# Optimization experiments

Measured on AMD Instinct MI355X. Metric: run time of the kernel, lower is better.

## Reference

```python
import jax, jax.numpy as jnp
import numpy as np

EPS = 1e-5

def bn_relu(x, g, b, leaky=0.0):
    # x: [B, C, N]; batch-norm over (batch, spatial) like torch train-mode BatchNorm1d
    m = x.mean((0, 2), keepdims=True)
    v = x.var((0, 2), keepdims=True)
    y = (x - m) * jax.lax.rsqrt(v + EPS) * g[None, :, None] + b[None, :, None]
    return jnp.where(y > 0, y, leaky * y)

def fps(xyz, npoint):
    # xyz: [B, N, 3] -> indices [B, npoint] (farthest point sampling, start at 0)
    B, N, _ = xyz.shape
    init_idx = jnp.zeros((B,), jnp.int32)
    d0 = jnp.full((B, N), 1e10, xyz.dtype)

    def step(carry, _):
        dists, last = carry
        p = jnp.take_along_axis(xyz, last[:, None, None], axis=1)  # [B,1,3]
        d = jnp.sum((xyz - p) ** 2, -1)                            # [B,N]
        dists = jnp.minimum(dists, d)
        nxt = jnp.argmax(dists, -1).astype(jnp.int32)
        return (dists, nxt), nxt

    (_, _), idxs = jax.lax.scan(step, (d0, init_idx), None, length=npoint - 1)
    return jnp.concatenate([init_idx[None, :], idxs], 0).T  # [B, npoint]

def sample_and_group(npoint, nsample, xyz, feat):
    # xyz: [B,N,3], feat: [B,N,C] -> new_xyz [B,S,3], new_feat [B,S,K,2C]
    fidx = fps(xyz, npoint)
    new_xyz = jnp.take_along_axis(xyz, fidx[:, :, None], axis=1)    # [B,S,3]
    center = jnp.take_along_axis(feat, fidx[:, :, None], axis=1)    # [B,S,C]
    # kNN of the S centers among all N points
    d = (jnp.sum(new_xyz ** 2, -1)[:, :, None]
         + jnp.sum(xyz ** 2, -1)[:, None, :]
         - 2.0 * jnp.einsum('bsc,bnc->bsn', new_xyz, xyz))          # [B,S,N]
    _, knn = jax.lax.top_k(-d, nsample)                              # [B,S,K]
    grouped = jnp.take_along_axis(feat[:, None, :, :], knn[..., None], axis=2)  # [B,S,K,C]
    gnorm = grouped - center[:, :, None, :]
    K = nsample
    new_feat = jnp.concatenate([gnorm, jnp.broadcast_to(center[:, :, None, :], gnorm.shape)], -1)
    return new_xyz, new_feat

def local_op(x, w1, g1, b1, w2, g2, b2):
    # x: [b, n, s, d] -> [b, out, n]
    b_, n, s, d = x.shape
    x = x.transpose(0, 1, 3, 2).reshape(b_ * n, d, s)   # [b*n, d, s]
    x1 = bn_relu(jnp.einsum('oc,bcs->bos', w1, x), g1, b1)
    x2 = bn_relu(jnp.einsum('oc,bcs->bos', w2, x1), g2, b2)
    x3 = x2.max(-1)                                      # adaptive_max_pool1d(.,1)
    return x3.reshape(b_, n, -1).transpose(0, 2, 1)

def setup_inputs() -> dict:
    key = jax.random.key(0)
    ks = jax.random.split(key, 16)
    f32 = jnp.float32
    B, N = 32, 1024
    inp = {
        'x': jax.random.normal(ks[0], (B, 6, N), f32),
        'w_c1': jax.random.normal(ks[1], (64, 6), f32) * 0.1,
        'g1': jnp.ones((64,), f32), 'b1': jnp.zeros((64,), f32),
        'w_c2': jax.random.normal(ks[2], (1024, 64), f32) * 0.05,
        'g2': jnp.ones((1024,), f32), 'b2': jnp.zeros((1024,), f32),
        'l0_w1': jax.random.normal(ks[3], (128, 128), f32) * 0.05,
        'l0_g1': jnp.ones((128,), f32), 'l0_b1': jnp.zeros((128,), f32),
        'l0_w2': jax.random.normal(ks[4], (128, 128), f32) * 0.05,
        'l0_g2': jnp.ones((128,), f32), 'l0_b2': jnp.zeros((128,), f32),
        'l1_w1': jax.random.normal(ks[5], (256, 256), f32) * 0.05,
        'l1_g1': jnp.ones((256,), f32), 'l1_b1': jnp.zeros((256,), f32),
        'l1_w2': jax.random.normal(ks[6], (256, 256), f32) * 0.05,
        'l1_g2': jnp.ones((256,), f32), 'l1_b2': jnp.zeros((256,), f32),
        'wf': jax.random.normal(ks[7], (512, 1280), f32) * 0.02,
        'gf': jnp.ones((512,), f32), 'bf': jnp.zeros((512,), f32),
    }
    return inp

def reference(x, w_c1, g1, b1, w_c2, g2, b2,
              l0_w1, l0_g1, l0_b1, l0_w2, l0_g2, l0_b2,
              l1_w1, l1_g1, l1_b1, l1_w2, l1_g2, l1_b2,
              wf, gf, bf):
    point_num = x.shape[2]
    stride = point_num // 256
    xyz = x[:, 0:3, :].transpose(0, 2, 1)                      # [B,N,3]
    h = bn_relu(jnp.einsum('oc,bcn->bon', w_c1, x), g1, b1)     # [B,64,N]
    x_skip = bn_relu(jnp.einsum('oc,bcn->bon', w_c2, h[:, :, ::stride]), g2, b2)  # [B,1024,256]
    feat = h.transpose(0, 2, 1)                                 # [B,N,64]
    new_xyz, nf = sample_and_group(512, 32, xyz, feat)          # nf: [B,512,32,128]
    f0 = local_op(nf, l0_w1, l0_g1, l0_b1, l0_w2, l0_g2, l0_b2) # [B,128,512]
    new_xyz, nf = sample_and_group(256, 32, new_xyz, f0.transpose(0, 2, 1))  # [B,256,32,256]
    f1 = local_op(nf, l1_w1, l1_g1, l1_b1, l1_w2, l1_g2, l1_b2) # [B,256,256]
    f1 = jnp.concatenate([f1, x_skip], 1)                        # [B,1280,256]
    res = bn_relu(jnp.einsum('oc,bcn->bon', wf, f1), gf, bf, leaky=0.2)  # [B,512,256]
    return res
```

## Files before the change

kernel.cpp:

```cpp
#include <hip/hip_runtime.h>
#include <stdint.h>

typedef unsigned int u32;
typedef unsigned short u16;
typedef __attribute__((ext_vector_type(8))) short bf16x8;
typedef __attribute__((ext_vector_type(4))) float f32x4;

#define DEV __device__ __forceinline__
#define BN_EPS 1e-5f

DEV float bf2f(u16 u){ return __uint_as_float(((u32)u) << 16); }
DEV u16 f2bf(float f){ u32 x = __float_as_uint(f); return (u16)((x + 0x7FFFu + ((x >> 16) & 1u)) >> 16); }

template<int CTRL, int RMASK, bool MAXOP>
DEV void dpp_step(float& d, u32& i){
  int ds = __float_as_int(d);
  int is = (int)i;
  int dn_ = __builtin_amdgcn_update_dpp(ds, ds, CTRL, RMASK, 0xf, false);
  int in_ = __builtin_amdgcn_update_dpp(is, is, CTRL, RMASK, 0xf, false);
  float dn = __int_as_float(dn_);
  u32 ii = (u32)in_;
  bool take = MAXOP ? (dn > d || (dn == d && ii < i))
                    : (dn < d || (dn == d && ii < i));
  if (take){ d = dn; i = ii; }
}

template<bool MAXOP>
DEV u32 dpp_arg_reduce(float& d, u32& i){
  dpp_step<0x111, 0xf, MAXOP>(d, i);
  dpp_step<0x112, 0xf, MAXOP>(d, i);
  dpp_step<0x114, 0xf, MAXOP>(d, i);
  dpp_step<0x118, 0xf, MAXOP>(d, i);
  dpp_step<0x142, 0xa, MAXOP>(d, i);
  dpp_step<0x143, 0xc, MAXOP>(d, i);
  return (u32)__builtin_amdgcn_readlane((int)i, 63);
}

__global__ void kfb(float* out, int n, float code){
  int i = blockIdx.x * 256 + threadIdx.x;
  if (i < n) out[i] = (i == 0) ? code : 0.f;
}

__global__ void kcast_bf(const float* __restrict__ src, int rows, int cols, int srcStride, int colOff,
                         u16* __restrict__ dst){
  int i = blockIdx.x * 256 + threadIdx.x;
  if (i >= rows * cols) return;
  int r = i / cols, c = i - r * cols;
  dst[r * cols + c] = f2bf(src[r * srcStride + colOff + c]);
}

__global__ __launch_bounds__(256) void kA_stats(const float* __restrict__ x, const float* __restrict__ w,
                                                const float* __restrict__ g, const float* __restrict__ b,
                                                float* __restrict__ sc, float* __restrict__ sh){
  int c = blockIdx.x, t = threadIdx.x;
  float wr[6];
#pragma unroll
  for (int j = 0; j < 6; ++j) wr[j] = w[c * 6 + j];
  float s = 0.f, ss = 0.f;
  for (int i = t; i < 32768; i += 256){
    int bb = i >> 10, n = i & 1023;
    const float* xb = x + bb * 6144 + n;
    float y = 0.f;
#pragma unroll
    for (int j = 0; j < 6; ++j) y += wr[j] * xb[j * 1024];
    s += y; ss += y * y;
  }
  __shared__ float rs[256], rq[256];
  rs[t] = s; rq[t] = ss; __syncthreads();
  for (int k = 128; k >= 1; k >>= 1){
    if (t < k){ rs[t] += rs[t + k]; rq[t] += rq[t + k]; }
    __syncthreads();
  }
  if (t == 0){
    float m = rs[0] * (1.f / 32768.f), e2 = rq[0] * (1.f / 32768.f);
    float var = e2 - m * m; if (var < 0.f) var = 0.f;
    float scv = g[c] * rsqrtf(var + BN_EPS);
    sc[c] = scv; sh[c] = b[c] - m * scv;
  }
}

__global__ __launch_bounds__(256) void kA_feat(const float* __restrict__ x, const float* __restrict__ w,
                                               const float* __restrict__ sc, const float* __restrict__ sh,
                                               u16* __restrict__ featT){
  int b = blockIdx.x >> 2, t = threadIdx.x;
  int n = ((blockIdx.x & 3) << 8) + t;
  __shared__ float wl[384], scl[64], shl[64];
  for (int u = t; u < 384; u += 256) wl[u] = w[u];
  if (t < 64){ scl[t] = sc[t]; shl[t] = sh[t]; }
  __syncthreads();
  float v[6];
  const float* xb = x + b * 6144 + n;
#pragma unroll
  for (int j = 0; j < 6; ++j) v[j] = xb[j * 1024];
  u32* row = (u32*)(featT + ((size_t)b * 1024 + n) * 64);
#pragma unroll
  for (int c2 = 0; c2 < 32; ++c2){
    float y0 = 0.f, y1 = 0.f;
#pragma unroll
    for (int j = 0; j < 6; ++j){
      y0 += wl[(2 * c2) * 6 + j] * v[j];
      y1 += wl[(2 * c2 + 1) * 6 + j] * v[j];
    }
    y0 = fmaxf(scl[2 * c2] * y0 + shl[2 * c2], 0.f);
    y1 = fmaxf(scl[2 * c2 + 1] * y1 + shl[2 * c2 + 1], 0.f);
    row[c2] = (u32)f2bf(y0) | ((u32)f2bf(y1) << 16);
  }
}

__global__ __launch_bounds__(256) void kxskip_pre(const u16* __restrict__ featT, const float* __restrict__ w2,
                                                  u16* __restrict__ xpre){
  int b = blockIdx.x >> 4, ot = blockIdx.x & 15, m = threadIdx.x;
  __shared__ float w2s[64][65];
  for (int u = threadIdx.x; u < 64 * 64; u += 256){
    int o = u >> 6, c = u & 63;
    w2s[o][c] = w2[(size_t)(ot * 64 + o) * 64 + c];
  }
  __syncthreads();
  float feat[64];
  const uint4* fr = (const uint4*)(featT + ((size_t)b * 1024 + 4 * m) * 64);
#pragma unroll
  for (int q = 0; q < 8; ++q){
    uint4 pv = fr[q];
    u32 wv[4] = {pv.x, pv.y, pv.z, pv.w};
#pragma unroll
    for (int h = 0; h < 4; ++h){
      feat[q * 8 + 2 * h]     = bf2f((u16)(wv[h] & 0xffff));
      feat[q * 8 + 2 * h + 1] = bf2f((u16)(wv[h] >> 16));
    }
  }
  u16* xb = xpre + ((size_t)b * 1024 + ot * 64) * 256 + m;
  for (int o = 0; o < 64; ++o){
    float acc = 0.f;
#pragma unroll
    for (int c = 0; c < 64; ++c) acc += w2s[o][c] * feat[c];
    xb[(size_t)o * 256] = f2bf(acc);
  }
}

__global__ __launch_bounds__(256) void kxskip_stats(const u16* __restrict__ xpre, const float* __restrict__ g,
                                                    const float* __restrict__ b, float* __restrict__ sc,
                                                    float* __restrict__ sh){
  int o = blockIdx.x, t = threadIdx.x;
  float s = 0.f, ss = 0.f;
  for (int i = t; i < 8192; i += 256){
    int bb = i >> 8, m = i & 255;
    float v = bf2f(xpre[((size_t)bb * 1024 + o) * 256 + m]);
    s += v; ss += v * v;
  }
  __shared__ float rs[256], rq[256];
  rs[t] = s; rq[t] = ss; __syncthreads();
  for (int k = 128; k >= 1; k >>= 1){
    if (t < k){ rs[t] += rs[t + k]; rq[t] += rq[t + k]; }
    __syncthreads();
  }
  if (t == 0){
    float m = rs[0] * (1.f / 8192.f), e2 = rq[0] * (1.f / 8192.f);
    float var = e2 - m * m; if (var < 0.f) var = 0.f;
    float scv = g[o] * rsqrtf(var + BN_EPS);
    sc[o] = scv; sh[o] = b[o] - m * scv;
  }
}

template<int NPTS, int NSAMP, int PSTRIDE>
__global__ __launch_bounds__(64) void kfps(const float* __restrict__ px_, const float* __restrict__ py_,
                                           const float* __restrict__ pz_, int bstride,
                                           int* __restrict__ fidx, float* __restrict__ nxyz){
  constexpr int PPL = NPTS / 64;
  __shared__ float sx[NPTS], sy[NPTS], sz[NPTS];
  int b = blockIdx.x, lane = threadIdx.x;
  float dd[PPL];
#pragma unroll
  for (int j = 0; j < PPL; ++j){
    int p = j * 64 + lane;
    sx[p] = px_[(size_t)b * bstride + p * PSTRIDE];
    sy[p] = py_[(size_t)b * bstride + p * PSTRIDE];
    sz[p] = pz_[(size_t)b * bstride + p * PSTRIDE];
    dd[j] = 1e10f;
  }
  __syncthreads();
  float cx = sx[0], cy = sy[0], cz = sz[0];
  if (lane == 0){
    fidx[(size_t)b * NSAMP] = 0;
    nxyz[(size_t)b * NSAMP * 3 + 0] = cx;
    nxyz[(size_t)b * NSAMP * 3 + 1] = cy;
    nxyz[(size_t)b * NSAMP * 3 + 2] = cz;
  }
  for (int s = 1; s < NSAMP; ++s){
    float bd = -1.f; u32 bi = 0;
#pragma unroll
    for (int j = 0; j < PPL; ++j){
      int p = j * 64 + lane;
      float dx = __fsub_rn(sx[p], cx);
      float dy = __fsub_rn(sy[p], cy);
      float dz = __fsub_rn(sz[p], cz);
      float d = __fadd_rn(__fadd_rn(__fmul_rn(dx, dx), __fmul_rn(dy, dy)), __fmul_rn(dz, dz));
      float v = fminf(dd[j], d);
      dd[j] = v;
      if (v > bd){ bd = v; bi = (u32)p; }
    }
    u32 win = dpp_arg_reduce<true>(bd, bi);
    cx = sx[win]; cy = sy[win]; cz = sz[win];
    if (lane == 0){
      fidx[(size_t)b * NSAMP + s] = (int)win;
      nxyz[((size_t)b * NSAMP + s) * 3 + 0] = cx;
      nxyz[((size_t)b * NSAMP + s) * 3 + 1] = cy;
      nxyz[((size_t)b * NSAMP + s) * 3 + 2] = cz;
    }
  }
}

template<int NPTS, int SOUT>
__global__ __launch_bounds__(256) void kknn(const float* __restrict__ px_, const float* __restrict__ py_,
                                            const float* __restrict__ pz_, int bstride, int pstride,
                                            const float* __restrict__ cxyz, int* __restrict__ knn){
  constexpr int PPL = NPTS / 64;
  int wid = blockIdx.x * 4 + (threadIdx.x >> 6);
  int lane = threadIdx.x & 63;
  int b = wid / SOUT, s = wid - b * SOUT;
  const float* cb = cxyz + ((size_t)b * SOUT + s) * 3;
  float cx = cb[0], cy = cb[1], cz = cb[2];
  float csq = __fadd_rn(__fadd_rn(__fmul_rn(cx, cx), __fmul_rn(cy, cy)), __fmul_rn(cz, cz));
  float kd[PPL];
#pragma unroll
  for (int j = 0; j < PPL; ++j){
    int p = j * 64 + lane;
    float xx = px_[(size_t)b * bstride + p * pstride];
    float yy = py_[(size_t)b * bstride + p * pstride];
    float zz = pz_[(size_t)b * bstride + p * pstride];
    float psq = __fadd_rn(__fadd_rn(__fmul_rn(xx, xx), __fmul_rn(yy, yy)), __fmul_rn(zz, zz));
    float dot = __fadd_rn(__fadd_rn(__fmul_rn(cx, xx), __fmul_rn(cy, yy)), __fmul_rn(cz, zz));
    kd[j] = __fsub_rn(__fadd_rn(csq, psq), __fmul_rn(2.f, dot));
  }
  int* outp = knn + ((size_t)b * SOUT + s) * 32;
  for (int k = 0; k < 32; ++k){
    float bd = kd[0]; u32 bi = (u32)lane;
#pragma unroll
    for (int j = 1; j < PPL; ++j){
      u32 p = (u32)(j * 64 + lane);
      if (kd[j] < bd){ bd = kd[j]; bi = p; }
    }
    u32 win = dpp_arg_reduce<false>(bd, bi);
    if (lane == 0) outp[k] = (int)win;
#pragma unroll
    for (int j = 0; j < PPL; ++j) if ((u32)(j * 64 + lane) == win) kd[j] = 3e38f;
  }
}

template<int CIN, int C, int NPTSRC, int SLOG>
__global__ __launch_bounds__(256) void kgm_pre(const u16* __restrict__ featSrc, const int* __restrict__ knnIdx,
                                               const int* __restrict__ fidx, const float* __restrict__ w1f,
                                               const u16* __restrict__ w1bf,
                                               u16* __restrict__ pre1, float* __restrict__ part){
  constexpr int MT  = C / 64;
  constexpr int KS1 = CIN / 32;
  constexpr int P1  = CIN + 8;
  int g = blockIdx.x, t = threadIdx.x, b = g >> SLOG;
  int l = t & 63, wv = t >> 6;
  int lg = l >> 4, ln = l & 15;

  __shared__ int   idxs[32];
  __shared__ float cen[CIN];
  __shared__ float bias[C];
  __shared__ u16   gsT[32][P1];

  if (t < 32) idxs[t] = knnIdx[(size_t)g * 32 + t];
  for (int u = t; u < CIN; u += 256) cen[u] = bf2f(featSrc[((size_t)(b * NPTSRC + fidx[g])) * CIN + u]);
  __syncthreads();

  for (int u = t; u < 32 * CIN / 8; u += 256){
    int k = u & 31, c8 = u >> 5;
    uint4 pv = *(const uint4*)(featSrc + ((size_t)(b * NPTSRC + idxs[k])) * CIN + c8 * 8);
    u32 wvv[4] = {pv.x, pv.y, pv.z, pv.w};
    u32 outw[4];
#pragma unroll
    for (int h = 0; h < 4; ++h){
      float a0 = bf2f((u16)(wvv[h] & 0xffff)) - cen[c8 * 8 + 2 * h];
      float a1 = bf2f((u16)(wvv[h] >> 16))    - cen[c8 * 8 + 2 * h + 1];
      outw[h] = (u32)f2bf(a0) | ((u32)f2bf(a1) << 16);
    }
    *(uint4*)&gsT[k][c8 * 8] = make_uint4(outw[0], outw[1], outw[2], outw[3]);
  }
  if (t < C){
    const float* wr = w1f + (size_t)t * (2 * CIN) + CIN;
    float bs = 0.f;
#pragma unroll 4
    for (int c = 0; c < CIN; ++c) bs += wr[c] * cen[c];
    bias[t] = bs;
  }
  __syncthreads();

  f32x4 acc[MT][2];
#pragma unroll
  for (int mt = 0; mt < MT; ++mt){ acc[mt][0] = (f32x4)0.f; acc[mt][1] = (f32x4)0.f; }
#pragma unroll
  for (int ks = 0; ks < KS1; ++ks){
    int c0 = ks * 32 + lg * 8;
    bf16x8 bfr0 = *(const bf16x8*)&gsT[ln][c0];
    bf16x8 bfr1 = *(const bf16x8*)&gsT[16 + ln][c0];
#pragma unroll
    for (int mt = 0; mt < MT; ++mt){
      int o0 = wv * (C / 4) + mt * 16;
      bf16x8 afr = *(const bf16x8*)(w1bf + (size_t)(o0 + ln) * CIN + c0);
      acc[mt][0] = __builtin_amdgcn_mfma_f32_16x16x32_bf16(afr, bfr0, acc[mt][0], 0, 0, 0);
      acc[mt][1] = __builtin_amdgcn_mfma_f32_16x16x32_bf16(afr, bfr1, acc[mt][1], 0, 0, 0);
    }
  }

#pragma unroll
  for (int mt = 0; mt < MT; ++mt){
    int obase = wv * (C / 4) + mt * 16 + lg * 4;
#pragma unroll
    for (int j = 0; j < 4; ++j){
      int o = obase + j;
      float bv = bias[o];
      float vA = acc[mt][0][j] + bv, vB = acc[mt][1][j] + bv;
      u16* pp = pre1 + ((size_t)g * C + o) * 32 + ln;
      pp[0]  = f2bf(vA);
      pp[16] = f2bf(vB);
      float s = vA + vB, ss = vA * vA + vB * vB;
#pragma unroll
      for (int mk = 1; mk < 16; mk <<= 1){ s += __shfl_xor(s, mk, 64); ss += __shfl_xor(ss, mk, 64); }
      if (ln == 0){
        part[((size_t)g * C + o) * 2 + 0] = s;
        part[((size_t)g * C + o) * 2 + 1] = ss;
      }
    }
  }
}

template<int C>
__global__ __launch_bounds__(256) void kgm_post(const u16* __restrict__ pre1,
                                                const float* __restrict__ sc1g, const float* __restrict__ sh1g,
                                                const u16* __restrict__ w2bf, const float* __restrict__ gp,
                                                float* __restrict__ part, float* __restrict__ pooledPre){
  constexpr int MT  = C / 64;
  constexpr int KS2 = C / 32;
  constexpr int P2  = C + 8;
  int g = blockIdx.x, t = threadIdx.x;
  int l = t & 63, wv = t >> 6;
  int lg = l >> 4, ln = l & 15;

  __shared__ u16   act2[32][P2];
  __shared__ float sc1s[C], sh1s[C];
  for (int u = t; u < C; u += 256){ sc1s[u] = sc1g[u]; sh1s[u] = sh1g[u]; }
  __syncthreads();

  for (int u = t; u < C * 4; u += 256){
    uint4 pv = *(const uint4*)(pre1 + (size_t)g * C * 32 + (size_t)u * 8);
    int o = u >> 2, k0 = (u & 3) << 3;
    float s1 = sc1s[o], h1 = sh1s[o];
    u32 wvv[4] = {pv.x, pv.y, pv.z, pv.w};
#pragma unroll
    for (int h = 0; h < 4; ++h){
      float a0 = fmaxf(s1 * bf2f((u16)(wvv[h] & 0xffff)) + h1, 0.f);
      float a1 = fmaxf(s1 * bf2f((u16)(wvv[h] >> 16))    + h1, 0.f);
      act2[k0 + 2 * h][o]     = f2bf(a0);
      act2[k0 + 2 * h + 1][o] = f2bf(a1);
    }
  }
  __syncthreads();

  f32x4 acc[MT][2];
#pragma unroll
  for (int mt = 0; mt < MT; ++mt){ acc[mt][0] = (f32x4)0.f; acc[mt][1] = (f32x4)0.f; }
#pragma unroll
  for (int ks = 0; ks < KS2; ++ks){
    int c0 = ks * 32 + lg * 8;
    bf16x8 bfr0 = *(const bf16x8*)&act2[ln][c0];
    bf16x8 bfr1 = *(const bf16x8*)&act2[16 + ln][c0];
#pragma unroll
    for (int mt = 0; mt < MT; ++mt){
      int o0 = wv * (C / 4) + mt * 16;
      bf16x8 afr = *(const bf16x8*)(w2bf + (size_t)(o0 + ln) * C + c0);
      acc[mt][0] = __builtin_amdgcn_mfma_f32_16x16x32_bf16(afr, bfr0, acc[mt][0], 0, 0, 0);
      acc[mt][1] = __builtin_amdgcn_mfma_f32_16x16x32_bf16(afr, bfr1, acc[mt][1], 0, 0, 0);
    }
  }

#pragma unroll
  for (int mt = 0; mt < MT; ++mt){
    int obase = wv * (C / 4) + mt * 16 + lg * 4;
#pragma unroll
    for (int j = 0; j < 4; ++j){
      float vA = acc[mt][0][j], vB = acc[mt][1][j];
      float s = vA + vB, ss = vA * vA + vB * vB;
      float mx = fmaxf(vA, vB), mn = fminf(vA, vB);
#pragma unroll
      for (int mk = 1; mk < 16; mk <<= 1){
        s += __shfl_xor(s, mk, 64); ss += __shfl_xor(ss, mk, 64);
        mx = fmaxf(mx, __shfl_xor(mx, mk, 64)); mn = fminf(mn, __shfl_xor(mn, mk, 64));
      }
      if (ln == 0){
        int o = obase + j;
        part[((size_t)g * C + o) * 2 + 0] = s;
        part[((size_t)g * C + o) * 2 + 1] = ss;
        pooledPre[(size_t)g * C + o] = (gp[o] >= 0.f) ? mx : mn;
      }
    }
  }
}

template<int C, int NG>
__global__ __launch_bounds__(256) void kstats_part(const float* __restrict__ part, const float* __restrict__ g_,
                                                   const float* __restrict__ b_, float* __restrict__ sc,
                                                   float* __restrict__ sh){
  int o = blockIdx.x, t = threadIdx.x;
  float s = 0.f, ss = 0.f;
  for (int i = t; i < NG; i += 256){
    s  += part[((size_t)i * C + o) * 2 + 0];
    ss += part[((size_t)i * C + o) * 2 + 1];
  }
  __shared__ float rs[256], rq[256];
  rs[t] = s; rq[t] = ss; __syncthreads();
  for (int k = 128; k >= 1; k >>= 1){
    if (t < k){ rs[t] += rs[t + k]; rq[t] += rq[t + k]; }
    __syncthreads();
  }
  if (t == 0){
    const float inv_n = 1.f / (float)(NG * 32);
    float m = rs[0] * inv_n, e2 = rq[0] * inv_n;
    float var = e2 - m * m; if (var < 0.f) var = 0.f;
    float scv = g_[o] * rsqrtf(var + BN_EPS);
    sc[o] = scv; sh[o] = b_[o] - m * scv;
  }
}

__global__ void kpool_fin1(const float* __restrict__ pooledPre, const float* __restrict__ sc,
                           const float* __restrict__ sh, u16* __restrict__ f0feat){
  int i = blockIdx.x * 256 + threadIdx.x;
  if (i >= 16384 * 128) return;
  int o = i & 127;
  float v = sc[o] * pooledPre[i] + sh[o];
  f0feat[i] = f2bf(fmaxf(v, 0.f));
}

__global__ void kpool_finT(const float* __restrict__ pooledPre, const float* __restrict__ sc,
                           const float* __restrict__ sh, u16* __restrict__ f1T){
  int i = blockIdx.x * 256 + threadIdx.x;
  if (i >= 8192 * 256) return;
  int gg = i >> 8, o = i & 255;
  int b = gg >> 8, s = gg & 255;
  float v = sc[o] * pooledPre[i] + sh[o];
  f1T[((size_t)(b * 256 + o)) * 256 + s] = f2bf(fmaxf(v, 0.f));
}

__global__ __launch_bounds__(256) void kfinal8(const u16* __restrict__ f1T, const u16* __restrict__ xpre,
                                               const float* __restrict__ scS, const float* __restrict__ shS,
                                               const float* __restrict__ wf, u16* __restrict__ finpre){
  int b = blockIdx.x >> 6, ot = blockIdx.x & 63, m = threadIdx.x;
  int o0 = ot * 8;
  const float* wb = wf + (size_t)o0 * 1280;
  float acc[8];
#pragma unroll
  for (int j = 0; j < 8; ++j) acc[j] = 0.f;
  const u16* fb = f1T + (size_t)b * 256 * 256 + m;
  for (int k = 0; k < 256; ++k){
    float v = bf2f(fb[(size_t)k * 256]);
#pragma unroll
    for (int j = 0; j < 8; ++j) acc[j] = fmaf(wb[(size_t)j * 1280 + k], v, acc[j]);
  }
  const u16* xb = xpre + (size_t)b * 1024 * 256 + m;
  for (int k = 0; k < 1024; ++k){
    float xv = bf2f(xb[(size_t)k * 256]);
    float v = fmaxf(scS[k] * xv + shS[k], 0.f);
#pragma unroll
    for (int j = 0; j < 8; ++j) acc[j] = fmaf(wb[(size_t)j * 1280 + 256 + k], v, acc[j]);
  }
#pragma unroll
  for (int j = 0; j < 8; ++j)
    finpre[((size_t)b * 512 + o0 + j) * 256 + m] = f2bf(acc[j]);
}

__global__ __launch_bounds__(256) void kstats_fin(const u16* __restrict__ finpre, const float* __restrict__ g,
                                                  const float* __restrict__ b, float* __restrict__ sc,
                                                  float* __restrict__ sh){
  int o = blockIdx.x, t = threadIdx.x;
  float s = 0.f, ss = 0.f;
  for (int i = t; i < 8192; i += 256){
    int bb = i >> 8, m = i & 255;
    float v = bf2f(finpre[((size_t)bb * 512 + o) * 256 + m]);
    s += v; ss += v * v;
  }
  __shared__ float rs[256], rq[256];
  rs[t] = s; rq[t] = ss; __syncthreads();
  for (int k = 128; k >= 1; k >>= 1){
    if (t < k){ rs[t] += rs[t + k]; rq[t] += rq[t + k]; }
    __syncthreads();
  }
  if (t == 0){
    float m = rs[0] * (1.f / 8192.f), e2 = rq[0] * (1.f / 8192.f);
    float var = e2 - m * m; if (var < 0.f) var = 0.f;
    float scv = g[o] * rsqrtf(var + BN_EPS);
    sc[o] = scv; sh[o] = b[o] - m * scv;
  }
}

__global__ void kapply(const u16* __restrict__ finpre, const float* __restrict__ sc,
                       const float* __restrict__ sh, float* __restrict__ out){
  int i = blockIdx.x * 256 + threadIdx.x;
  if (i >= 32 * 512 * 256) return;
  int o = (i >> 8) & 511;
  float v = sc[o] * bf2f(finpre[i]) + sh[o];
  out[i] = v > 0.f ? v : 0.2f * v;
}

extern "C" void kernel_launch(void* const* d_in, const int* in_sizes, int n_in,
                              void* d_out, int out_size, void* d_ws, size_t ws_size,
                              hipStream_t stream){
  const float* x    = (const float*)d_in[0];
  const float* w_c1 = (const float*)d_in[1];
  const float* g1   = (const float*)d_in[2];
  const float* b1   = (const float*)d_in[3];
  const float* w_c2 = (const float*)d_in[4];
  const float* g2   = (const float*)d_in[5];
  const float* b2   = (const float*)d_in[6];
  const float* l0w1 = (const float*)d_in[7];
  const float* l0g1 = (const float*)d_in[8];
  const float* l0b1 = (const float*)d_in[9];
  const float* l0w2 = (const float*)d_in[10];
  const float* l0g2 = (const float*)d_in[11];
  const float* l0b2 = (const float*)d_in[12];
  const float* l1w1 = (const float*)d_in[13];
  const float* l1g1 = (const float*)d_in[14];
  const float* l1b1 = (const float*)d_in[15];
  const float* l1w2 = (const float*)d_in[16];
  const float* l1g2 = (const float*)d_in[17];
  const float* l1b2 = (const float*)d_in[18];
  const float* wf   = (const float*)d_in[19];
  const float* gf   = (const float*)d_in[20];
  const float* bfp  = (const float*)d_in[21];
  float* out = (float*)d_out;

  char* ws = (char*)d_ws;
  size_t cur = 0;
  auto alloc = [&](size_t bytes) -> char* {
    char* p = ws + cur;
    cur += (bytes + 255) & ~(size_t)255;
    return p;
  };
  float* sc1  = (float*)alloc(64 * 4);    float* sh1  = (float*)alloc(64 * 4);
  float* scSK = (float*)alloc(1024 * 4);  float* shSK = (float*)alloc(1024 * 4);
  float* scA1 = (float*)alloc(128 * 4);   float* shA1 = (float*)alloc(128 * 4);
  float* scA2 = (float*)alloc(128 * 4);   float* shA2 = (float*)alloc(128 * 4);
  float* scC1 = (float*)alloc(256 * 4);   float* shC1 = (float*)alloc(256 * 4);
  float* scC2 = (float*)alloc(256 * 4);   float* shC2 = (float*)alloc(256 * 4);
  float* scF  = (float*)alloc(512 * 4);   float* shF  = (float*)alloc(512 * 4);
  u16* w1bf1 = (u16*)alloc((size_t)128 * 64 * 2);
  u16* w2bf1 = (u16*)alloc((size_t)128 * 128 * 2);
  u16* w1bf2 = (u16*)alloc((size_t)256 * 128 * 2);
  u16* w2bf2 = (u16*)alloc((size_t)256 * 256 * 2);
  u16*   featT  = (u16*)  alloc((size_t)32 * 1024 * 64 * 2);
  u16*   xpre   = (u16*)  alloc((size_t)32 * 1024 * 256 * 2);
  int*   fidx1  = (int*)  alloc((size_t)32 * 512 * 4);
  float* nxyz1  = (float*)alloc((size_t)32 * 512 * 3 * 4);
  int*   knn1   = (int*)  alloc((size_t)32 * 512 * 32 * 4);
  int*   fidx2  = (int*)  alloc((size_t)32 * 256 * 4);
  float* nxyz2  = (float*)alloc((size_t)32 * 256 * 3 * 4);
  int*   knn2   = (int*)  alloc((size_t)32 * 256 * 32 * 4);
  u16*   pre1   = (u16*)  alloc((size_t)16384 * 128 * 32 * 2);
  float* part   = (float*)alloc((size_t)16384 * 128 * 2 * 4);
  float* pooledPre = (float*)alloc((size_t)16384 * 128 * 4);
  u16*   f0feat = (u16*)  alloc((size_t)16384 * 128 * 2);
  u16*   f1T    = (u16*)  alloc((size_t)32 * 256 * 256 * 2);
  u16*   finpre = (u16*)  alloc((size_t)32 * 512 * 256 * 2);

  if (cur > ws_size){
    float code = -1000.f - (float)(ws_size >> 20);
    kfb<<<(out_size + 255) / 256, 256, 0, stream>>>(out, out_size, code);
    return;
  }

  kcast_bf<<<(128 * 64 + 255) / 256, 256, 0, stream>>>(l0w1, 128, 64, 128, 0, w1bf1);
  kcast_bf<<<(128 * 128 + 255) / 256, 256, 0, stream>>>(l0w2, 128, 128, 128, 0, w2bf1);
  kcast_bf<<<(256 * 128 + 255) / 256, 256, 0, stream>>>(l1w1, 256, 128, 256, 0, w1bf2);
  kcast_bf<<<(256 * 256 + 255) / 256, 256, 0, stream>>>(l1w2, 256, 256, 256, 0, w2bf2);

  kA_stats<<<64, 256, 0, stream>>>(x, w_c1, g1, b1, sc1, sh1);
  kA_feat<<<128, 256, 0, stream>>>(x, w_c1, sc1, sh1, featT);

  kxskip_pre<<<512, 256, 0, stream>>>(featT, w_c2, xpre);
  kxskip_stats<<<1024, 256, 0, stream>>>(xpre, g2, b2, scSK, shSK);

  kfps<1024, 512, 1><<<32, 64, 0, stream>>>(x, x + 1024, x + 2048, 6144, fidx1, nxyz1);
  kknn<1024, 512><<<32 * 512 / 4, 256, 0, stream>>>(x, x + 1024, x + 2048, 6144, 1, nxyz1, knn1);

  kgm_pre<64, 128, 1024, 9><<<16384, 256, 0, stream>>>(featT, knn1, fidx1, l0w1, w1bf1, pre1, part);
  kstats_part<128, 16384><<<128, 256, 0, stream>>>(part, l0g1, l0b1, scA1, shA1);
  kgm_post<128><<<16384, 256, 0, stream>>>(pre1, scA1, shA1, w2bf1, l0g2, part, pooledPre);
  kstats_part<128, 16384><<<128, 256, 0, stream>>>(part, l0g2, l0b2, scA2, shA2);
  kpool_fin1<<<8192, 256, 0, stream>>>(pooledPre, scA2, shA2, f0feat);

  kfps<512, 256, 3><<<32, 64, 0, stream>>>(nxyz1, nxyz1 + 1, nxyz1 + 2, 1536, fidx2, nxyz2);
  kknn<512, 256><<<32 * 256 / 4, 256, 0, stream>>>(nxyz1, nxyz1 + 1, nxyz1 + 2, 1536, 3, nxyz2, knn2);

  kgm_pre<128, 256, 512, 8><<<8192, 256, 0, stream>>>(f0feat, knn2, fidx2, l1w1, w1bf2, pre1, part);
  kstats_part<256, 8192><<<256, 256, 0, stream>>>(part, l1g1, l1b1, scC1, shC1);
  kgm_post<256><<<8192, 256, 0, stream>>>(pre1, scC1, shC1, w2bf2, l1g2, part, pooledPre);
  kstats_part<256, 8192><<<256, 256, 0, stream>>>(part, l1g2, l1b2, scC2, shC2);
  kpool_finT<<<8192, 256, 0, stream>>>(pooledPre, scC2, shC2, f1T);

  kfinal8<<<2048, 256, 0, stream>>>(f1T, xpre, scSK, shSK, wf, finpre);
  kstats_fin<<<512, 256, 0, stream>>>(finpre, gf, bfp, scF, shF);
  kapply<<<16384, 256, 0, stream>>>(finpre, scF, shF, out);
}
```

Measured before the change: 1.818 ms.

## Spread farthest point sampling across four waves per batch with cross-wave argmax

The FPS kernel now runs one 256-thread block per batch instead of a single 64-lane wave, so each lane handles a quarter as many points per iteration. Each wave does a DPP argmax reduction, and the four wave results are merged through double-buffered shared memory with one barrier per sample step. Points are stored as float4 in shared memory so each point is read with a single load. The serial per-step cost shrinks, but a block barrier is added on every sampled point, which could eat part of the gain for the smaller 512-point stage.

```diff
diff --git a/kernel.cpp b/kernel.cpp
--- a/kernel.cpp
+++ b/kernel.cpp
@@ -26,14 +26,22 @@
 }
 
 template<bool MAXOP>
-DEV u32 dpp_arg_reduce(float& d, u32& i){
+DEV void dpp_arg_reduce_vi(float& d, u32& i, float& outd, u32& outi){
   dpp_step<0x111, 0xf, MAXOP>(d, i);
   dpp_step<0x112, 0xf, MAXOP>(d, i);
   dpp_step<0x114, 0xf, MAXOP>(d, i);
   dpp_step<0x118, 0xf, MAXOP>(d, i);
   dpp_step<0x142, 0xa, MAXOP>(d, i);
   dpp_step<0x143, 0xc, MAXOP>(d, i);
-  return (u32)__builtin_amdgcn_readlane((int)i, 63);
+  outi = (u32)__builtin_amdgcn_readlane((int)i, 63);
+  outd = __int_as_float(__builtin_amdgcn_readlane(__float_as_int(d), 63));
+}
+
+template<bool MAXOP>
+DEV u32 dpp_arg_reduce(float& d, u32& i){
+  float od; u32 oi;
+  dpp_arg_reduce_vi<MAXOP>(d, i, od, oi);
+  return oi;
 }
 
 __global__ void kfb(float* out, int n, float code){
@@ -162,50 +170,67 @@
 }
 
 template<int NPTS, int NSAMP, int PSTRIDE>
-__global__ __launch_bounds__(64) void kfps(const float* __restrict__ px_, const float* __restrict__ py_,
-                                           const float* __restrict__ pz_, int bstride,
-                                           int* __restrict__ fidx, float* __restrict__ nxyz){
-  constexpr int PPL = NPTS / 64;
-  __shared__ float sx[NPTS], sy[NPTS], sz[NPTS];
-  int b = blockIdx.x, lane = threadIdx.x;
+__global__ __launch_bounds__(256) void kfps4(const float* __restrict__ px_, const float* __restrict__ py_,
+                                             const float* __restrict__ pz_, int bstride,
+                                             int* __restrict__ fidx, float* __restrict__ nxyz){
+  constexpr int PPL = NPTS / 256;
+  __shared__ float4 pts[NPTS];
+  __shared__ float rbd[2][4];
+  __shared__ u32   rbi[2][4];
+  int b = blockIdx.x, t = threadIdx.x;
+  int wv = t >> 6;
   float dd[PPL];
 #pragma unroll
   for (int j = 0; j < PPL; ++j){
-    int p = j * 64 + lane;
-    sx[p] = px_[(size_t)b * bstride + p * PSTRIDE];
-    sy[p] = py_[(size_t)b * bstride + p * PSTRIDE];
-    sz[p] = pz_[(size_t)b * bstride + p * PSTRIDE];
+    int p = j * 256 + t;
+    pts[p] = make_float4(px_[(size_t)b * bstride + p * PSTRIDE],
+                         py_[(size_t)b * bstride + p * PSTRIDE],
+                         pz_[(size_t)b * bstride + p * PSTRIDE], 0.f);
     dd[j] = 1e10f;
   }
   __syncthreads();
-  float cx = sx[0], cy = sy[0], cz = sz[0];
-  if (lane == 0){
+  float4 c0 = pts[0];
+  float cx = c0.x, cy = c0.y, cz = c0.z;
+  if (t == 0){
     fidx[(size_t)b * NSAMP] = 0;
     nxyz[(size_t)b * NSAMP * 3 + 0] = cx;
     nxyz[(size_t)b * NSAMP * 3 + 1] = cy;
     nxyz[(size_t)b * NSAMP * 3 + 2] = cz;
   }
+  int buf = 0;
   for (int s = 1; s < NSAMP; ++s){
     float bd = -1.f; u32 bi = 0;
 #pragma unroll
     for (int j = 0; j < PPL; ++j){
-      int p = j * 64 + lane;
-      float dx = __fsub_rn(sx[p], cx);
-      float dy = __fsub_rn(sy[p], cy);
-      float dz = __fsub_rn(sz[p], cz);
+      int p = j * 256 + t;
+      float4 pt = pts[p];
+      float dx = __fsub_rn(pt.x, cx);
+      float dy = __fsub_rn(pt.y, cy);
+      float dz = __fsub_rn(pt.z, cz);
       float d = __fadd_rn(__fadd_rn(__fmul_rn(dx, dx), __fmul_rn(dy, dy)), __fmul_rn(dz, dz));
       float v = fminf(dd[j], d);
       dd[j] = v;
       if (v > bd){ bd = v; bi = (u32)p; }
     }
-    u32 win = dpp_arg_reduce<true>(bd, bi);
-    cx = sx[win]; cy = sy[win]; cz = sz[win];
-    if (lane == 0){
-      fidx[(size_t)b * NSAMP + s] = (int)win;
+    float wbd; u32 wbi;
+    dpp_arg_reduce_vi<true>(bd, bi, wbd, wbi);
+    if ((t & 63) == 0){ rbd[buf][wv] = wbd; rbi[buf][wv] = wbi; }
+    __syncthreads();
+    float Bd = rbd[buf][0]; u32 Bi = rbi[buf][0];
+#pragma unroll
+    for (int w = 1; w < 4; ++w){
+      float od = rbd[buf][w]; u32 oi = rbi[buf][w];
+      if (od > Bd || (od == Bd && oi < Bi)){ Bd = od; Bi = oi; }
+    }
+    float4 cw = pts[Bi];
+    cx = cw.x; cy = cw.y; cz = cw.z;
+    if (t == 0){
+      fidx[(size_t)b * NSAMP + s] = (int)Bi;
       nxyz[((size_t)b * NSAMP + s) * 3 + 0] = cx;
       nxyz[((size_t)b * NSAMP + s) * 3 + 1] = cy;
       nxyz[((size_t)b * NSAMP + s) * 3 + 2] = cz;
     }
+    buf ^= 1;
   }
 }
 
@@ -581,7 +606,7 @@
   kxskip_pre<<<512, 256, 0, stream>>>(featT, w_c2, xpre);
   kxskip_stats<<<1024, 256, 0, stream>>>(xpre, g2, b2, scSK, shSK);
 
-  kfps<1024, 512, 1><<<32, 64, 0, stream>>>(x, x + 1024, x + 2048, 6144, fidx1, nxyz1);
+  kfps4<1024, 512, 1><<<32, 256, 0, stream>>>(x, x + 1024, x + 2048, 6144, fidx1, nxyz1);
   kknn<1024, 512><<<32 * 512 / 4, 256, 0, stream>>>(x, x + 1024, x + 2048, 6144, 1, nxyz1, knn1);
 
   kgm_pre<64, 128, 1024, 9><<<16384, 256, 0, stream>>>(featT, knn1, fidx1, l0w1, w1bf1, pre1, part);
@@ -590,7 +615,7 @@
   kstats_part<128, 16384><<<128, 256, 0, stream>>>(part, l0g2, l0b2, scA2, shA2);
   kpool_fin1<<<8192, 256, 0, stream>>>(pooledPre, scA2, shA2, f0feat);
 
-  kfps<512, 256, 3><<<32, 64, 0, stream>>>(nxyz1, nxyz1 + 1, nxyz1 + 2, 1536, fidx2, nxyz2);
+  kfps4<512, 256, 3><<<32, 256, 0, stream>>>(nxyz1, nxyz1 + 1, nxyz1 + 2, 1536, fidx2, nxyz2);
   kknn<512, 256><<<32 * 256 / 4, 256, 0, stream>>>(nxyz1, nxyz1 + 1, nxyz1 + 2, 1536, 3, nxyz2, knn2);
 
   kgm_pre<128, 256, 512, 8><<<8192, 256, 0, stream>>>(f0feat, knn2, fidx2, l1w1, w1bf2, pre1, part);
```

After: 1.926 ms. 6.0% more time.

## Overlap serial FPS with independent GEMM work via fused launches; cheaper DPP argmax

Applied to the files above, without the earlier changes.

The two farthest-point-sampling passes, which are serial single-wave loops on 32 blocks, now share a launch with independent work: the first FPS runs alongside the x_skip projection, and the second FPS runs alongside the first grouped-MLP pre-activation kernel. Because FPS2 depends only on nxyz1, it can start early instead of waiting behind stage-0 work. The DPP argmax/argmin reduction is rewritten as a float max/min reduction, a readlane broadcast, and then a min-index reduction, replacing paired compare-and-select steps. In exchange, FPS blocks now hold 256-thread slots with 192 idle threads, and the kgm_pre body shares a kernel with the FPS shared-memory footprint, which may reduce occupancy for the large grid.

```diff
diff --git a/kernel.cpp b/kernel.cpp
--- a/kernel.cpp
+++ b/kernel.cpp
@@ -12,28 +12,43 @@
 DEV float bf2f(u16 u){ return __uint_as_float(((u32)u) << 16); }
 DEV u16 f2bf(float f){ u32 x = __float_as_uint(f); return (u16)((x + 0x7FFFu + ((x >> 16) & 1u)) >> 16); }
 
-template<int CTRL, int RMASK, bool MAXOP>
-DEV void dpp_step(float& d, u32& i){
-  int ds = __float_as_int(d);
-  int is = (int)i;
-  int dn_ = __builtin_amdgcn_update_dpp(ds, ds, CTRL, RMASK, 0xf, false);
-  int in_ = __builtin_amdgcn_update_dpp(is, is, CTRL, RMASK, 0xf, false);
-  float dn = __int_as_float(dn_);
-  u32 ii = (u32)in_;
-  bool take = MAXOP ? (dn > d || (dn == d && ii < i))
-                    : (dn < d || (dn == d && ii < i));
-  if (take){ d = dn; i = ii; }
+template<int CTRL, int RMASK>
+DEV float dppf(float v){
+  int r = __builtin_amdgcn_update_dpp(__float_as_int(v), __float_as_int(v), CTRL, RMASK, 0xf, false);
+  return __int_as_float(r);
+}
+template<int CTRL, int RMASK>
+DEV u32 dppu(u32 v){
+  return (u32)__builtin_amdgcn_update_dpp((int)v, (int)v, CTRL, RMASK, 0xf, false);
 }
 
 template<bool MAXOP>
-DEV u32 dpp_arg_reduce(float& d, u32& i){
-  dpp_step<0x111, 0xf, MAXOP>(d, i);
-  dpp_step<0x112, 0xf, MAXOP>(d, i);
-  dpp_step<0x114, 0xf, MAXOP>(d, i);
-  dpp_step<0x118, 0xf, MAXOP>(d, i);
-  dpp_step<0x142, 0xa, MAXOP>(d, i);
-  dpp_step<0x143, 0xc, MAXOP>(d, i);
-  return (u32)__builtin_amdgcn_readlane((int)i, 63);
+DEV u32 arg_reduce2(float bd, u32 bi){
+  float m = bd;
+  if (MAXOP){
+    m = fmaxf(m, dppf<0x111, 0xf>(m));
+    m = fmaxf(m, dppf<0x112, 0xf>(m));
+    m = fmaxf(m, dppf<0x114, 0xf>(m));
+    m = fmaxf(m, dppf<0x118, 0xf>(m));
+    m = fmaxf(m, dppf<0x142, 0xa>(m));
+    m = fmaxf(m, dppf<0x143, 0xc>(m));
+  } else {
+    m = fminf(m, dppf<0x111, 0xf>(m));
+    m = fminf(m, dppf<0x112, 0xf>(m));
+    m = fminf(m, dppf<0x114, 0xf>(m));
+    m = fminf(m, dppf<0x118, 0xf>(m));
+    m = fminf(m, dppf<0x142, 0xa>(m));
+    m = fminf(m, dppf<0x143, 0xc>(m));
+  }
+  float M = __int_as_float(__builtin_amdgcn_readlane(__float_as_int(m), 63));
+  u32 key = (bd == M) ? bi : 0xFFFFFFFFu;
+  key = min(key, dppu<0x111, 0xf>(key));
+  key = min(key, dppu<0x112, 0xf>(key));
+  key = min(key, dppu<0x114, 0xf>(key));
+  key = min(key, dppu<0x118, 0xf>(key));
+  key = min(key, dppu<0x142, 0xa>(key));
+  key = min(key, dppu<0x143, 0xc>(key));
+  return (u32)__builtin_amdgcn_readlane((int)key, 63);
 }
 
 __global__ void kfb(float* out, int n, float code){
@@ -107,9 +122,58 @@
   }
 }
 
-__global__ __launch_bounds__(256) void kxskip_pre(const u16* __restrict__ featT, const float* __restrict__ w2,
-                                                  u16* __restrict__ xpre){
-  int b = blockIdx.x >> 4, ot = blockIdx.x & 15, m = threadIdx.x;
+template<int NPTS, int NSAMP, int PSTRIDE>
+DEV void fps_body(const float* __restrict__ px_, const float* __restrict__ py_,
+                  const float* __restrict__ pz_, int bstride,
+                  int* __restrict__ fidx, float* __restrict__ nxyz, int b){
+  constexpr int PPL = NPTS / 64;
+  __shared__ float sx[NPTS], sy[NPTS], sz[NPTS];
+  int t = threadIdx.x;
+  for (int p = t; p < NPTS; p += 256){
+    sx[p] = px_[(size_t)b * bstride + p * PSTRIDE];
+    sy[p] = py_[(size_t)b * bstride + p * PSTRIDE];
+    sz[p] = pz_[(size_t)b * bstride + p * PSTRIDE];
+  }
+  __syncthreads();
+  if (t >= 64) return;
+  int lane = t;
+  float dd[PPL];
+#pragma unroll
+  for (int j = 0; j < PPL; ++j) dd[j] = 1e10f;
+  float cx = sx[0], cy = sy[0], cz = sz[0];
+  if (lane == 0){
+    fidx[(size_t)b * NSAMP] = 0;
+    nxyz[(size_t)b * NSAMP * 3 + 0] = cx;
+    nxyz[(size_t)b * NSAMP * 3 + 1] = cy;
+    nxyz[(size_t)b * NSAMP * 3 + 2] = cz;
+  }
+  for (int s = 1; s < NSAMP; ++s){
+    float bd = -1.f; u32 bi = 0;
+#pragma unroll
+    for (int j = 0; j < PPL; ++j){
+      int p = j * 64 + lane;
+      float dx = __fsub_rn(sx[p], cx);
+      float dy = __fsub_rn(sy[p], cy);
+      float dz = __fsub_rn(sz[p], cz);
+      float d = __fadd_rn(__fadd_rn(__fmul_rn(dx, dx), __fmul_rn(dy, dy)), __fmul_rn(dz, dz));
+      float v = fminf(dd[j], d);
+      dd[j] = v;
+      if (v > bd){ bd = v; bi = (u32)p; }
+    }
+    u32 win = arg_reduce2<true>(bd, bi);
+    cx = sx[win]; cy = sy[win]; cz = sz[win];
+    if (lane == 0){
+      fidx[(size_t)b * NSAMP + s] = (int)win;
+      nxyz[((size_t)b * NSAMP + s) * 3 + 0] = cx;
+      nxyz[((size_t)b * NSAMP + s) * 3 + 1] = cy;
+      nxyz[((size_t)b * NSAMP + s) * 3 + 2] = cz;
+    }
+  }
+}
+
+DEV void xskip_body(const u16* __restrict__ featT, const float* __restrict__ w2,
+                    u16* __restrict__ xpre, int bi){
+  int b = bi >> 4, ot = bi & 15, m = threadIdx.x;
   __shared__ float w2s[64][65];
   for (int u = threadIdx.x; u < 64 * 64; u += 256){
     int o = u >> 6, c = u & 63;
@@ -134,6 +198,17 @@
 #pragma unroll
     for (int c = 0; c < 64; ++c) acc += w2s[o][c] * feat[c];
     xb[(size_t)o * 256] = f2bf(acc);
+  }
+}
+
+__global__ __launch_bounds__(256) void kfused1(const float* __restrict__ x,
+                                               const u16* __restrict__ featT, const float* __restrict__ w2,
+                                               u16* __restrict__ xpre,
+                                               int* __restrict__ fidx1, float* __restrict__ nxyz1){
+  if (blockIdx.x < 32){
+    fps_body<1024, 512, 1>(x, x + 1024, x + 2048, 6144, fidx1, nxyz1, blockIdx.x);
+  } else {
+    xskip_body(featT, w2, xpre, blockIdx.x - 32);
   }
 }
 
@@ -158,54 +233,6 @@
     float var = e2 - m * m; if (var < 0.f) var = 0.f;
     float scv = g[o] * rsqrtf(var + BN_EPS);
     sc[o] = scv; sh[o] = b[o] - m * scv;
-  }
-}
-
-template<int NPTS, int NSAMP, int PSTRIDE>
-__global__ __launch_bounds__(64) void kfps(const float* __restrict__ px_, const float* __restrict__ py_,
-                                           const float* __restrict__ pz_, int bstride,
-                                           int* __restrict__ fidx, float* __restrict__ nxyz){
-  constexpr int PPL = NPTS / 64;
-  __shared__ float sx[NPTS], sy[NPTS], sz[NPTS];
-  int b = blockIdx.x, lane = threadIdx.x;
-  float dd[PPL];
-#pragma unroll
-  for (int j = 0; j < PPL; ++j){
-    int p = j * 64 + lane;
-    sx[p] = px_[(size_t)b * bstride + p * PSTRIDE];
-    sy[p] = py_[(size_t)b * bstride + p * PSTRIDE];
-    sz[p] = pz_[(size_t)b * bstride + p * PSTRIDE];
-    dd[j] = 1e10f;
-  }
-  __syncthreads();
-  float cx = sx[0], cy = sy[0], cz = sz[0];
-  if (lane == 0){
-    fidx[(size_t)b * NSAMP] = 0;
-    nxyz[(size_t)b * NSAMP * 3 + 0] = cx;
-    nxyz[(size_t)b * NSAMP * 3 + 1] = cy;
-    nxyz[(size_t)b * NSAMP * 3 + 2] = cz;
-  }
-  for (int s = 1; s < NSAMP; ++s){
-    float bd = -1.f; u32 bi = 0;
-#pragma unroll
-    for (int j = 0; j < PPL; ++j){
-      int p = j * 64 + lane;
-      float dx = __fsub_rn(sx[p], cx);
-      float dy = __fsub_rn(sy[p], cy);
-      float dz = __fsub_rn(sz[p], cz);
-      float d = __fadd_rn(__fadd_rn(__fmul_rn(dx, dx), __fmul_rn(dy, dy)), __fmul_rn(dz, dz));
-      float v = fminf(dd[j], d);
-      dd[j] = v;
-      if (v > bd){ bd = v; bi = (u32)p; }
-    }
-    u32 win = dpp_arg_reduce<true>(bd, bi);
-    cx = sx[win]; cy = sy[win]; cz = sz[win];
-    if (lane == 0){
-      fidx[(size_t)b * NSAMP + s] = (int)win;
-      nxyz[((size_t)b * NSAMP + s) * 3 + 0] = cx;
-      nxyz[((size_t)b * NSAMP + s) * 3 + 1] = cy;
-      nxyz[((size_t)b * NSAMP + s) * 3 + 2] = cz;
-    }
   }
 }
 
@@ -239,7 +266,7 @@
       u32 p = (u32)(j * 64 + lane);
       if (kd[j] < bd){ bd = kd[j]; bi = p; }
     }
-    u32 win = dpp_arg_reduce<false>(bd, bi);
+    u32 win = arg_reduce2<false>(bd, bi);
     if (lane == 0) outp[k] = (int)win;
 #pragma unroll
     for (int j = 0; j < PPL; ++j) if ((u32)(j * 64 + lane) == win) kd[j] = 3e38f;
@@ -247,14 +274,14 @@
 }
 
 template<int CIN, int C, int NPTSRC, int SLOG>
-__global__ __launch_bounds__(256) void kgm_pre(const u16* __restrict__ featSrc, const int* __restrict__ knnIdx,
-                                               const int* __restrict__ fidx, const float* __restrict__ w1f,
-                                               const u16* __restrict__ w1bf,
-                                               u16* __restrict__ pre1, float* __restrict__ part){
+DEV void kgm_pre_body(const u16* __restrict__ featSrc, const int* __restrict__ knnIdx,
+                      const int* __restrict__ fidx, const float* __restrict__ w1f,
+                      const u16* __restrict__ w1bf,
+                      u16* __restrict__ pre1, float* __restrict__ part, int g){
   constexpr int MT  = C / 64;
   constexpr int KS1 = CIN / 32;
   constexpr int P1  = CIN + 8;
-  int g = blockIdx.x, t = threadIdx.x, b = g >> SLOG;
+  int t = threadIdx.x, b = g >> SLOG;
   int l = t & 63, wv = t >> 6;
   int lg = l >> 4, ln = l & 15;
 
@@ -325,6 +352,27 @@
         part[((size_t)g * C + o) * 2 + 1] = ss;
       }
     }
+  }
+}
+
+template<int CIN, int C, int NPTSRC, int SLOG>
+__global__ __launch_bounds__(256) void kgm_pre(const u16* __restrict__ featSrc, const int* __restrict__ knnIdx,
+                                               const int* __restrict__ fidx, const float* __restrict__ w1f,
+                                               const u16* __restrict__ w1bf,
+                                               u16* __restrict__ pre1, float* __restrict__ part){
+  kgm_pre_body<CIN, C, NPTSRC, SLOG>(featSrc, knnIdx, fidx, w1f, w1bf, pre1, part, blockIdx.x);
+}
+
+__global__ __launch_bounds__(256) void kfused2(const float* __restrict__ nxyz1_,
+                                               int* __restrict__ fidx2, float* __restrict__ nxyz2,
+                                               const u16* __restrict__ featT, const int* __restrict__ knn1,
+                                               const int* __restrict__ fidx1, const float* __restrict__ l0w1,
+                                               const u16* __restrict__ w1bf1,
+                                               u16* __restrict__ pre1, float* __restrict__ part){
+  if (blockIdx.x < 32){
+    fps_body<512, 256, 3>(nxyz1_, nxyz1_ + 1, nxyz1_ + 2, 1536, fidx2, nxyz2, blockIdx.x);
+  } else {
+    kgm_pre_body<64, 128, 1024, 9>(featT, knn1, fidx1, l0w1, w1bf1, pre1, part, blockIdx.x - 32);
   }
 }
 
@@ -578,19 +626,18 @@
   kA_stats<<<64, 256, 0, stream>>>(x, w_c1, g1, b1, sc1, sh1);
   kA_feat<<<128, 256, 0, stream>>>(x, w_c1, sc1, sh1, featT);
 
-  kxskip_pre<<<512, 256, 0, stream>>>(featT, w_c2, xpre);
+  kfused1<<<544, 256, 0, stream>>>(x, featT, w_c2, xpre, fidx1, nxyz1);
   kxskip_stats<<<1024, 256, 0, stream>>>(xpre, g2, b2, scSK, shSK);
 
-  kfps<1024, 512, 1><<<32, 64, 0, stream>>>(x, x + 1024, x + 2048, 6144, fidx1, nxyz1);
   kknn<1024, 512><<<32 * 512 / 4, 256, 0, stream>>>(x, x + 1024, x + 2048, 6144, 1, nxyz1, knn1);
 
-  kgm_pre<64, 128, 1024, 9><<<16384, 256, 0, stream>>>(featT, knn1, fidx1, l0w1, w1bf1, pre1, part);
+  kfused2<<<32 + 16384, 256, 0, stream>>>(nxyz1, fidx2, nxyz2,
+                                          featT, knn1, fidx1, l0w1, w1bf1, pre1, part);
   kstats_part<128, 16384><<<128, 256, 0, stream>>>(part, l0g1, l0b1, scA1, shA1);
   kgm_post<128><<<16384, 256, 0, stream>>>(pre1, scA1, shA1, w2bf1, l0g2, part, pooledPre);
   kstats_part<128, 16384><<<128, 256, 0, stream>>>(part, l0g2, l0b2, scA2, shA2);
   kpool_fin1<<<8192, 256, 0, stream>>>(pooledPre, scA2, shA2, f0feat);
 
-  kfps<512, 256, 3><<<32, 64, 0, stream>>>(nxyz1, nxyz1 + 1, nxyz1 + 2, 1536, fidx2, nxyz2);
   kknn<512, 256><<<32 * 256 / 4, 256, 0, stream>>>(nxyz1, nxyz1 + 1, nxyz1 + 2, 1536, 3, nxyz2, knn2);
 
   kgm_pre<128, 256, 512, 8><<<8192, 256, 0, stream>>>(f0feat, knn2, fidx2, l1w1, w1bf2, pre1, part);
```

After: 1.560 ms. 1.17x faster.
